# Kernel tuning notes

Measured on AMD Instinct MI355X. Metric: run time of the kernel, lower is better.

The kernel has to match this reference:

```python
import jax, jax.numpy as jnp
import numpy as np

QUANT_DEPTH = 4
EMBED_DIM = 256
N_EMBED = 8192
B, H, W = 8, 32, 32


def setup_inputs() -> dict:
    key = jax.random.key(0)
    k1, k2 = jax.random.split(key)
    x = jax.random.normal(k1, (B, H, W, EMBED_DIM), dtype=jnp.float32)
    codebooks = jax.random.normal(k2, (QUANT_DEPTH, N_EMBED, EMBED_DIM), dtype=jnp.float32)
    return {"x": x, "codebooks": codebooks}


def _nearest_code(flat, cb):
    # flat: [N, D], cb: [K, D] -> idx: [N]
    # ||v - c||^2 = ||v||^2 + ||c||^2 - 2 v.c  (addmm in torch source)
    d = (jnp.sum(flat * flat, axis=1, keepdims=True)
         + jnp.sum(cb * cb, axis=1)[None, :]
         - 2.0 * (flat @ cb.T))  # [N, K]
    return jnp.argmin(d, axis=1)


def reference(x, codebooks):
    Bx, h, w, D = x.shape
    # quantization path is entirely non-differentiable (torch: detach + no_grad)
    resid = jax.lax.stop_gradient(x)
    agg = jnp.zeros_like(resid)
    quant_list = []
    code_list = []
    for i in range(codebooks.shape[0]):
        cb = codebooks[i]                      # [K, D]
        idx = _nearest_code(resid.reshape(-1, D), cb)  # [N]
        quant = cb[idx].reshape(Bx, h, w, D)
        resid = resid - quant
        agg = agg + quant
        quant_list.append(agg)
        code_list.append(idx.reshape(Bx, h, w, 1))
    codes = jnp.concatenate(code_list, axis=-1)  # [B, h, w, depth]
    # commitment loss: mean over depths of mean((x - agg_i.detach())^2)
    commitment_loss = jnp.mean(
        jnp.stack([jnp.mean((x - jax.lax.stop_gradient(q)) ** 2) for q in quant_list]))
    # straight-through estimator
    quants_trunc = x + jax.lax.stop_gradient(quant_list[-1] - x)
    return quants_trunc, commitment_loss, codes
```

## Files before the change

### kernel.cpp

```cpp
#include <hip/hip_runtime.h>

#define DIM   256
#define NVEC  8192
#define NCODE 8192
#define DEPTH 4

#define KBLK  16
#define KC    (NCODE / KBLK)
#define FCAP  8192
#define FKS   32
#define FV    8
#define KAPPA 0.025f

typedef short  b8 __attribute__((ext_vector_type(8)));
typedef short  b4 __attribute__((ext_vector_type(4)));
typedef float  f4 __attribute__((ext_vector_type(4)));

static __device__ __forceinline__ unsigned short f2bf(float f) {
  unsigned u = __float_as_uint(f);
  return (unsigned short)((u + 0x7FFFu + ((u >> 16) & 1u)) >> 16);
}

static __device__ __forceinline__ void gll16(const void* g, void* l) {
  __builtin_amdgcn_global_load_lds(
      (const __attribute__((address_space(1))) void*)g,
      (__attribute__((address_space(3))) void*)l, 16, 0, 0);
}

__global__ __launch_bounds__(256) void prep_norms(const float* __restrict__ cb_all,
                                                  float* __restrict__ cc,
                                                  float* __restrict__ cchat) {
  int row  = blockIdx.x * 4 + (threadIdx.x >> 6);
  int lane = threadIdx.x & 63;
  float4 v = *(const float4*)&cb_all[(size_t)row * DIM + lane * 4];
  float st = 0.f, sh = 0.f;
  float vv[4] = {v.x, v.y, v.z, v.w};
  #pragma unroll
  for (int j = 0; j < 4; ++j) {
    float hf = __uint_as_float(((unsigned)f2bf(vv[j])) << 16);
    st += vv[j] * vv[j];
    sh += hf * hf;
  }
  #pragma unroll
  for (int off = 32; off > 0; off >>= 1) {
    st += __shfl_down(st, off, 64);
    sh += __shfl_down(sh, off, 64);
  }
  if (lane == 0) { cc[row] = st; cchat[row] = sh; }
}

__global__ __launch_bounds__(256) void prep_depth(const float* __restrict__ cbd,
                                                  unsigned short* __restrict__ cbh,
                                                  float* __restrict__ cbT) {
  __shared__ float ts[64][68];
  const int kb = blockIdx.x >> 2, db = blockIdx.x & 3;
  const int k0 = kb * 64, d0 = db * 64;
  const int t  = threadIdx.x;
  const int r  = t >> 2;
  const int c4 = (t & 3) * 16;

  const float* src = cbd + (size_t)(k0 + r) * DIM + d0 + c4;
  float4 q[4];
  #pragma unroll
  for (int i = 0; i < 4; ++i) q[i] = *(const float4*)(src + i * 4);

  b8 h0, h1;
  #pragma unroll
  for (int j = 0; j < 4; ++j) { h0[j] = (short)f2bf(q[0][j]); h0[4 + j] = (short)f2bf(q[1][j]); }
  #pragma unroll
  for (int j = 0; j < 4; ++j) { h1[j] = (short)f2bf(q[2][j]); h1[4 + j] = (short)f2bf(q[3][j]); }
  *(b8*)&cbh[(size_t)(k0 + r) * DIM + d0 + c4]     = h0;
  *(b8*)&cbh[(size_t)(k0 + r) * DIM + d0 + c4 + 8] = h1;

  #pragma unroll
  for (int i = 0; i < 4; ++i)
    #pragma unroll
    for (int j = 0; j < 4; ++j)
      ts[c4 + i * 4 + j][r] = q[i][j];
  __syncthreads();

  const int dd = t >> 2, kk4 = (t & 3) * 16;
  float* dst = cbT + (size_t)(d0 + dd) * NCODE + k0 + kk4;
  #pragma unroll
  for (int q4 = 0; q4 < 4; ++q4)
    *(float4*)(dst + q4 * 4) = *(const float4*)&ts[dd][kk4 + q4 * 4];
}

__global__ __launch_bounds__(256) void init_kernel(const float* __restrict__ x,
                                                   float* __restrict__ resid,
                                                   unsigned short* __restrict__ rb,
                                                   float* __restrict__ rsum0) {
  int n    = blockIdx.x * 4 + (threadIdx.x >> 6);
  int lane = threadIdx.x & 63;
  float4 v = *(const float4*)&x[(size_t)n * DIM + lane * 4];
  *(float4*)&resid[(size_t)n * DIM + lane * 4] = v;
  b4 hv; hv[0] = (short)f2bf(v.x); hv[1] = (short)f2bf(v.y);
  hv[2] = (short)f2bf(v.z); hv[3] = (short)f2bf(v.w);
  *(b4*)&rb[(size_t)n * DIM + lane * 4] = hv;
  float s = v.x * v.x + v.y * v.y + v.z * v.z + v.w * v.w;
  #pragma unroll
  for (int off = 32; off > 0; off >>= 1) s += __shfl_down(s, off, 64);
  if (lane == 0) rsum0[n] = s;
}

__global__ __launch_bounds__(512, 4) void coarse_kernel(
    const unsigned short* __restrict__ rb,
    const unsigned short* __restrict__ cbh,
    const float* __restrict__ cchat,
    float* __restrict__ pv1, int* __restrict__ pi1, float* __restrict__ pv2,
    int* __restrict__ fcount) {
  __shared__ __align__(16) char lds[65536];

  const int tid  = threadIdx.x;
  const int w    = tid >> 6;
  const int l    = tid & 63;
  const int mw   = w >> 1, kw = w & 1;
  const int mblk = blockIdx.x / KBLK;
  const int kblk = blockIdx.x % KBLK;
  const int m0   = mblk * 128;
  const int K0   = kblk * KC;

  if (blockIdx.x == 0 && tid == 0) *fcount = 0;

  int aoff[2], boff[2], ldst[2];
  #pragma unroll
  for (int it = 0; it < 2; ++it) {
    int o = it * 512 + tid;
    int row = o >> 3, ssl = (o & 7) ^ (row & 7);
    aoff[it] = (m0 + row) * 512 + ssl * 16;
    boff[it] = (K0 + row) * 512 + ssl * 16;
    ldst[it] = o * 16;
  }
  int offA[2][2], offB[4][2];
  #pragma unroll
  for (int mf = 0; mf < 2; ++mf) {
    int row = mw * 32 + mf * 16 + (l & 15);
    int base = row * 128 + (((l >> 4) ^ (row & 7)) * 16);
    offA[mf][0] = base; offA[mf][1] = base ^ 64;
  }
  #pragma unroll
  for (int nf = 0; nf < 4; ++nf) {
    int row = kw * 64 + nf * 16 + (l & 15);
    int base = row * 128 + (((l >> 4) ^ (row & 7)) * 16);
    offB[nf][0] = base; offB[nf][1] = base ^ 64;
  }

  const int kgb = K0 + kw * 64 + (l & 15);

  float tv1[8], tv2[8];
  int   ti1[8];
  #pragma unroll
  for (int s = 0; s < 8; ++s) { tv1[s] = 3.4e38f; tv2[s] = 3.4e38f; ti1[s] = 0; }

  f4 acc[2][4];

  #pragma unroll
  for (int it = 0; it < 2; ++it) {
    gll16((const char*)rb  + aoff[it], lds + ldst[it]);
    gll16((const char*)cbh + boff[it], lds + 16384 + ldst[it]);
  }
  __syncthreads();

  #pragma unroll 2
  for (int p = 0; p < 16; ++p) {
    const int buf = p & 1;
    const int kt  = p >> 2, dt = p & 3;
    if (p < 15) {
      const int np = p + 1;
      const int nb = np & 1, nkt = np >> 2, ndt = np & 3;
      #pragma unroll
      for (int it = 0; it < 2; ++it) {
        gll16((const char*)rb  + aoff[it] + ndt * 128,
              lds + nb * 32768 + ldst[it]);
        gll16((const char*)cbh + boff[it] + nkt * 65536 + ndt * 128,
              lds + nb * 32768 + 16384 + ldst[it]);
      }
    }
    if (dt == 0) {
      #pragma unroll
      for (int i = 0; i < 2; ++i)
        #pragma unroll
        for (int j = 0; j < 4; ++j)
          acc[i][j] = (f4){0.f, 0.f, 0.f, 0.f};
    }
    #pragma unroll
    for (int kk = 0; kk < 2; ++kk) {
      b8 af[2], bb[4];
      #pragma unroll
      for (int mf = 0; mf < 2; ++mf)
        af[mf] = *(const b8*)(lds + buf * 32768 + offA[mf][kk]);
      #pragma unroll
      for (int nf = 0; nf < 4; ++nf)
        bb[nf] = *(const b8*)(lds + buf * 32768 + 16384 + offB[nf][kk]);
      #pragma unroll
      for (int mf = 0; mf < 2; ++mf)
        #pragma unroll
        for (int nf = 0; nf < 4; ++nf)
          acc[mf][nf] = __builtin_amdgcn_mfma_f32_16x16x32_bf16(
              af[mf], bb[nf], acc[mf][nf], 0, 0, 0);
    }
    if (dt == 3) {
      float cn[4]; int kg[4];
      #pragma unroll
      for (int nf = 0; nf < 4; ++nf) {
        kg[nf] = kgb + kt * 128 + nf * 16;
        cn[nf] = cchat[kg[nf]];
      }
      #pragma unroll
      for (int mf = 0; mf < 2; ++mf)
        #pragma unroll
        for (int r = 0; r < 4; ++r) {
          const int s0 = mf * 4 + r;
          #pragma unroll
          for (int nf = 0; nf < 4; ++nf) {
            float s = fmaf(-2.f, acc[mf][nf][r], cn[nf]);
            bool  c = s < tv1[s0];
            float m2 = fminf(tv2[s0], s);
            tv2[s0] = c ? tv1[s0] : m2;
            ti1[s0] = c ? kg[nf] : ti1[s0];
            tv1[s0] = c ? s : tv1[s0];
          }
        }
    }
    __syncthreads();
  }

  float* Mv1 = (float*)lds;
  int*   Mi1 = (int*)(lds + 1024);
  float* Mv2 = (float*)(lds + 2048);

  #pragma unroll
  for (int s0 = 0; s0 < 8; ++s0) {
    float v1 = tv1[s0], v2 = tv2[s0];
    int   i1 = ti1[s0];
    #pragma unroll
    for (int m = 1; m < 16; m <<= 1) {
      float qv1 = __shfl_xor(v1, m);
      int   qi1 = __shfl_xor(i1, m);
      float qv2 = __shfl_xor(v2, m);
      bool  qw  = (qv1 < v1) || (qv1 == v1 && qi1 < i1);
      float lose = qw ? v1 : qv1;
      float wv2  = qw ? qv2 : v2;
      v2 = fminf(wv2, lose);
      if (qw) { v1 = qv1; i1 = qi1; }
    }
    if ((l & 15) == 0) {
      int mf = s0 >> 2, r = s0 & 3;
      int rowL = mw * 32 + mf * 16 + (l >> 4) * 4 + r;
      Mv1[rowL * 2 + kw] = v1; Mi1[rowL * 2 + kw] = i1; Mv2[rowL * 2 + kw] = v2;
    }
  }
  __syncthreads();
  if (tid < 128) {
    float a1 = Mv1[tid * 2],     a2 = Mv2[tid * 2];     int a1i = Mi1[tid * 2];
    float b1 = Mv1[tid * 2 + 1], b2 = Mv2[tid * 2 + 1]; int b1i = Mi1[tid * 2 + 1];
    bool  bw = (b1 < a1) || (b1 == a1 && b1i < a1i);
    float v1 = bw ? b1 : a1; int i1 = bw ? b1i : a1i;
    float v2 = fminf(bw ? b2 : a2, bw ? a1 : b1);
    int n = m0 + tid;
    pv1[kblk * NVEC + n] = v1;
    pi1[kblk * NVEC + n] = i1;
    pv2[kblk * NVEC + n] = v2;
  }
}

__global__ __launch_bounds__(256) void merge_kernel(
    const float* __restrict__ pv1, const int* __restrict__ pi1,
    const float* __restrict__ pv2, const float* __restrict__ vnorm,
    int* __restrict__ idx, int* __restrict__ flist, int* __restrict__ fslot,
    int* __restrict__ fcount) {
  int n = blockIdx.x * 256 + threadIdx.x;
  float v1 = 3.4e38f, v2 = 3.4e38f; int i1 = 0;
  #pragma unroll
  for (int kb = 0; kb < KBLK; ++kb) {
    float b1 = pv1[kb * NVEC + n]; int b1i = pi1[kb * NVEC + n];
    float b2 = pv2[kb * NVEC + n];
    bool  bw = (b1 < v1) || (b1 == v1 && b1i < i1);
    float lose = bw ? v1 : b1;
    float wv2  = bw ? b2 : v2;
    v2 = fminf(wv2, lose);
    if (bw) { v1 = b1; i1 = b1i; }
  }
  idx[n] = i1;
  float thr = KAPPA * sqrtf(fmaxf(v1 + vnorm[n], 0.f)) + 1e-5f;
  int slot = -1;
  if (v2 - v1 < thr) {
    slot = atomicAdd(fcount, 1);
    flist[slot] = n;
  }
  fslot[n] = slot;
}

__global__ __launch_bounds__(256, 4) void fb_scan_t(
    const float* __restrict__ cbT, const float* __restrict__ cc,
    const float* __restrict__ resid, const int* __restrict__ flist,
    const int* __restrict__ fcount,
    float* __restrict__ fpv, int* __restrict__ fpi) {
  __shared__ float vsT[DIM][FV + 4];
  __shared__ float mv[FV][4];
  __shared__ int   mi[FV][4];
  const int cnt = min(*fcount, FCAP);
  const int ks = blockIdx.x & (FKS - 1);
  const int t = threadIdx.x;
  const int w = t >> 6, l = t & 63;
  const int k = ks * 256 + t;
  const float cn = cc[k];

  for (int chunk = blockIdx.x >> 5; chunk * FV < cnt; chunk += 256) {
    __syncthreads();
    #pragma unroll
    for (int v = 0; v < FV; ++v) {
      int s = chunk * FV + v;
      int n = flist[s < cnt ? s : chunk * FV];
      vsT[t][v] = resid[(size_t)n * DIM + t];
    }
    __syncthreads();

    float dot[FV];
    #pragma unroll
    for (int v = 0; v < FV; ++v) dot[v] = 0.f;

    #pragma unroll 8
    for (int d = 0; d < DIM; ++d) {
      float cv = cbT[(size_t)d * NCODE + k];
      f4 a0 = *(const f4*)&vsT[d][0];
      f4 a1 = *(const f4*)&vsT[d][4];
      dot[0] = fmaf(cv, a0[0], dot[0]);
      dot[1] = fmaf(cv, a0[1], dot[1]);
      dot[2] = fmaf(cv, a0[2], dot[2]);
      dot[3] = fmaf(cv, a0[3], dot[3]);
      dot[4] = fmaf(cv, a1[0], dot[4]);
      dot[5] = fmaf(cv, a1[1], dot[5]);
      dot[6] = fmaf(cv, a1[2], dot[6]);
      dot[7] = fmaf(cv, a1[3], dot[7]);
    }

    #pragma unroll
    for (int v = 0; v < FV; ++v) {
      float bv = fmaf(-2.f, dot[v], cn);
      int   bi = k;
      #pragma unroll
      for (int m = 1; m < 64; m <<= 1) {
        float qv = __shfl_xor(bv, m);
        int   qi = __shfl_xor(bi, m);
        if (qv < bv || (qv == bv && qi < bi)) { bv = qv; bi = qi; }
      }
      if (l == 0) { mv[v][w] = bv; mi[v][w] = bi; }
    }
    __syncthreads();
    if (t < FV) {
      float bv = mv[t][0]; int bi = mi[t][0];
      #pragma unroll
      for (int ww = 1; ww < 4; ++ww) {
        float qv = mv[t][ww]; int qi = mi[t][ww];
        if (qv < bv || (qv == bv && qi < bi)) { bv = qv; bi = qi; }
      }
      if (chunk * FV + t < cnt) {
        fpv[(size_t)(chunk * FV + t) * FKS + ks] = bv;
        fpi[(size_t)(chunk * FV + t) * FKS + ks] = bi;
      }
    }
  }
}

__global__ __launch_bounds__(256) void update_kernel(
    const float* __restrict__ cb, const int* __restrict__ idx,
    const int* __restrict__ fslot,
    const float* __restrict__ fpv, const int* __restrict__ fpi,
    float* __restrict__ resid, unsigned short* __restrict__ rb,
    float* __restrict__ rsum_out, float* __restrict__ codes_out, int depth) {
  int n    = blockIdx.x * 4 + (threadIdx.x >> 6);
  int lane = threadIdx.x & 63;
  int s    = fslot[n];
  int bi;
  if (s >= 0) {
    float v = 3.4e38f; int ii = 0x7fffffff;
    if (lane < FKS) { v = fpv[(size_t)s * FKS + lane]; ii = fpi[(size_t)s * FKS + lane]; }
    #pragma unroll
    for (int m = 1; m < FKS; m <<= 1) {
      float qv = __shfl_xor(v, m);
      int   qi = __shfl_xor(ii, m);
      if (qv < v || (qv == v && qi < ii)) { v = qv; ii = qi; }
    }
    bi = __shfl(ii, 0, 64);
  } else {
    bi = idx[n];
  }
  float4 q = *(const float4*)&cb[(size_t)bi * DIM + lane * 4];
  float4 r = *(float4*)&resid[(size_t)n * DIM + lane * 4];
  r.x -= q.x; r.y -= q.y; r.z -= q.z; r.w -= q.w;
  *(float4*)&resid[(size_t)n * DIM + lane * 4] = r;
  b4 hv; hv[0] = (short)f2bf(r.x); hv[1] = (short)f2bf(r.y);
  hv[2] = (short)f2bf(r.z); hv[3] = (short)f2bf(r.w);
  *(b4*)&rb[(size_t)n * DIM + lane * 4] = hv;
  float s2 = r.x * r.x + r.y * r.y + r.z * r.z + r.w * r.w;
  #pragma unroll
  for (int off = 32; off > 0; off >>= 1) s2 += __shfl_down(s2, off, 64);
  if (lane == 0) {
    rsum_out[n] = s2;
    codes_out[n * DEPTH + depth] = (float)bi;
  }
}

__global__ __launch_bounds__(256) void finalize(const float* __restrict__ x,
                                                float* __restrict__ out,
                                                const float* __restrict__ rsumL) {
  int i = blockIdx.x * blockDim.x + threadIdx.x;
  float4 r  = *(float4*)&out[(size_t)i * 4];
  float4 xv = *(const float4*)&x[(size_t)i * 4];
  float4 o;
  o.x = xv.x - r.x; o.y = xv.y - r.y; o.z = xv.z - r.z; o.w = xv.w - r.w;
  *(float4*)&out[(size_t)i * 4] = o;

  if (blockIdx.x == 0) {
    __shared__ float sm[256];
    float s = 0.f;
    for (int j = threadIdx.x; j < DEPTH * NVEC; j += 256) s += rsumL[j];
    sm[threadIdx.x] = s;
    __syncthreads();
    for (int off = 128; off > 0; off >>= 1) {
      if (threadIdx.x < off) sm[threadIdx.x] += sm[threadIdx.x + off];
      __syncthreads();
    }
    if (threadIdx.x == 0)
      out[NVEC * DIM] = sm[0] / (float)DEPTH / (float)(NVEC * DIM);
  }
}

extern "C" void kernel_launch(void* const* d_in, const int* in_sizes, int n_in,
                              void* d_out, int out_size, void* d_ws, size_t ws_size,
                              hipStream_t stream) {
  const float* x  = (const float*)d_in[0];
  const float* cb = (const float*)d_in[1];
  float* out = (float*)d_out;
  char*  wsb = (char*)d_ws;

  unsigned short* cbh = (unsigned short*)(wsb);
  unsigned short* rb  = (unsigned short*)(wsb + 4194304);
  float* cbT   = (float*)(wsb + 8388608);
  float* cc    = (float*)(wsb + 16777216);
  float* cchat = (float*)(wsb + 16908288);
  float* pv1   = (float*)(wsb + 17039360);
  int*   pi1   = (int*)  (wsb + 17563648);
  float* pv2   = (float*)(wsb + 18087936);
  float* rsum  = (float*)(wsb + 18612224);
  int*   idx   = (int*)  (wsb + 18776064);
  int*   flist = (int*)  (wsb + 18808832);
  int*   fslot = (int*)  (wsb + 18841600);
  int*   fcount= (int*)  (wsb + 18874368);
  float* fpv   = (float*)(wsb + 18878464);
  int*   fpi   = (int*)  (wsb + 19927040);

  float* resid     = out;
  float* codes_out = out + NVEC * DIM + 1;

  prep_norms<<<(DEPTH * NCODE) / 4, 256, 0, stream>>>(cb, cc, cchat);
  init_kernel<<<NVEC / 4, 256, 0, stream>>>(x, resid, rb, rsum);

  for (int d = 0; d < DEPTH; ++d) {
    const size_t cbo = (size_t)d * NCODE * DIM;
    prep_depth<<<512, 256, 0, stream>>>(cb + cbo, cbh, cbT);
    coarse_kernel<<<(NVEC / 128) * KBLK, 512, 0, stream>>>(
        rb, cbh, cchat + d * NCODE, pv1, pi1, pv2, fcount);
    merge_kernel<<<NVEC / 256, 256, 0, stream>>>(
        pv1, pi1, pv2, rsum + d * NVEC, idx, flist, fslot, fcount);
    fb_scan_t<<<256 * FKS, 256, 0, stream>>>(
        cbT, cc + d * NCODE, resid, flist, fcount, fpv, fpi);
    update_kernel<<<NVEC / 4, 256, 0, stream>>>(
        cb + cbo, idx, fslot, fpv, fpi, resid, rb,
        rsum + (d + 1) * NVEC, codes_out, d);
  }
  finalize<<<(NVEC * DIM / 4) / 256, 256, 0, stream>>>(x, out, rsum + NVEC);
}
```

Measured before the change: 528.2 us.

## Keep residual A fragments in registers and halve code-block split count

```diff
diff --git a/kernel.cpp b/kernel.cpp
--- a/kernel.cpp
+++ b/kernel.cpp
@@ -5,8 +5,9 @@
 #define NCODE 8192
 #define DEPTH 4
 
-#define KBLK  16
+#define KBLK  8
 #define KC    (NCODE / KBLK)
+#define KT    (KC / 128)
 #define FCAP  8192
 #define FKS   32
 #define FV    8
@@ -153,6 +154,7 @@
   for (int s = 0; s < 8; ++s) { tv1[s] = 3.4e38f; tv2[s] = 3.4e38f; ti1[s] = 0; }
 
   f4 acc[2][4];
+  b8 ar[4][2][2];
 
   #pragma unroll
   for (int it = 0; it < 2; ++it) {
@@ -161,68 +163,80 @@
   }
   __syncthreads();
 
-  #pragma unroll 2
-  for (int p = 0; p < 16; ++p) {
-    const int buf = p & 1;
-    const int kt  = p >> 2, dt = p & 3;
-    if (p < 15) {
-      const int np = p + 1;
-      const int nb = np & 1, nkt = np >> 2, ndt = np & 3;
+  for (int kt = 0; kt < KT; ++kt) {
+    #pragma unroll
+    for (int dt = 0; dt < 4; ++dt) {
+      const int buf = dt & 1;
+      if (!(kt == KT - 1 && dt == 3)) {
+        const int ndt = (dt + 1) & 3;
+        const int nb  = ndt & 1;
+        const int nktoff = (dt == 3) ? (kt + 1) * 65536 : kt * 65536;
+        if (kt == 0 && dt < 3) {
+          #pragma unroll
+          for (int it = 0; it < 2; ++it)
+            gll16((const char*)rb + aoff[it] + ndt * 128,
+                  lds + nb * 32768 + ldst[it]);
+        }
+        #pragma unroll
+        for (int it = 0; it < 2; ++it)
+          gll16((const char*)cbh + boff[it] + nktoff + ndt * 128,
+                lds + nb * 32768 + 16384 + ldst[it]);
+      }
+      if (dt == 0) {
+        #pragma unroll
+        for (int i = 0; i < 2; ++i)
+          #pragma unroll
+          for (int j = 0; j < 4; ++j)
+            acc[i][j] = (f4){0.f, 0.f, 0.f, 0.f};
+      }
       #pragma unroll
-      for (int it = 0; it < 2; ++it) {
-        gll16((const char*)rb  + aoff[it] + ndt * 128,
-              lds + nb * 32768 + ldst[it]);
-        gll16((const char*)cbh + boff[it] + nkt * 65536 + ndt * 128,
-              lds + nb * 32768 + 16384 + ldst[it]);
-      }
-    }
-    if (dt == 0) {
-      #pragma unroll
-      for (int i = 0; i < 2; ++i)
-        #pragma unroll
-        for (int j = 0; j < 4; ++j)
-          acc[i][j] = (f4){0.f, 0.f, 0.f, 0.f};
-    }
-    #pragma unroll
-    for (int kk = 0; kk < 2; ++kk) {
-      b8 af[2], bb[4];
-      #pragma unroll
-      for (int mf = 0; mf < 2; ++mf)
-        af[mf] = *(const b8*)(lds + buf * 32768 + offA[mf][kk]);
-      #pragma unroll
-      for (int nf = 0; nf < 4; ++nf)
-        bb[nf] = *(const b8*)(lds + buf * 32768 + 16384 + offB[nf][kk]);
-      #pragma unroll
-      for (int mf = 0; mf < 2; ++mf)
+      for (int kk = 0; kk < 2; ++kk) {
+        b8 af[2], bb[4];
+        if (kt == 0) {
+          #pragma unroll
+          for (int mf = 0; mf < 2; ++mf) {
+            af[mf] = *(const b8*)(lds + buf * 32768 + offA[mf][kk]);
+            ar[dt][kk][mf] = af[mf];
+          }
+        } else {
+          #pragma unroll
+          for (int mf = 0; mf < 2; ++mf) af[mf] = ar[dt][kk][mf];
+        }
         #pragma unroll
         for (int nf = 0; nf < 4; ++nf)
-          acc[mf][nf] = __builtin_amdgcn_mfma_f32_16x16x32_bf16(
-              af[mf], bb[nf], acc[mf][nf], 0, 0, 0);
-    }
-    if (dt == 3) {
-      float cn[4]; int kg[4];
-      #pragma unroll
-      for (int nf = 0; nf < 4; ++nf) {
-        kg[nf] = kgb + kt * 128 + nf * 16;
-        cn[nf] = cchat[kg[nf]];
-      }
-      #pragma unroll
-      for (int mf = 0; mf < 2; ++mf)
-        #pragma unroll
-        for (int r = 0; r < 4; ++r) {
-          const int s0 = mf * 4 + r;
-          #pragma unroll
-          for (int nf = 0; nf < 4; ++nf) {
-            float s = fmaf(-2.f, acc[mf][nf][r], cn[nf]);
-            bool  c = s < tv1[s0];
-            float m2 = fminf(tv2[s0], s);
-            tv2[s0] = c ? tv1[s0] : m2;
-            ti1[s0] = c ? kg[nf] : ti1[s0];
-            tv1[s0] = c ? s : tv1[s0];
+          bb[nf] = *(const b8*)(lds + buf * 32768 + 16384 + offB[nf][kk]);
+        #pragma unroll
+        for (int mf = 0; mf < 2; ++mf)
+          #pragma unroll
+          for (int nf = 0; nf < 4; ++nf)
+            acc[mf][nf] = __builtin_amdgcn_mfma_f32_16x16x32_bf16(
+                af[mf], bb[nf], acc[mf][nf], 0, 0, 0);
+      }
+      if (dt == 3) {
+        float cn[4]; int kg[4];
+        #pragma unroll
+        for (int nf = 0; nf < 4; ++nf) {
+          kg[nf] = kgb + kt * 128 + nf * 16;
+          cn[nf] = cchat[kg[nf]];
+        }
+        #pragma unroll
+        for (int mf = 0; mf < 2; ++mf)
+          #pragma unroll
+          for (int r = 0; r < 4; ++r) {
+            const int s0 = mf * 4 + r;
+            #pragma unroll
+            for (int nf = 0; nf < 4; ++nf) {
+              float s = fmaf(-2.f, acc[mf][nf][r], cn[nf]);
+              bool  c = s < tv1[s0];
+              float m2 = fminf(tv2[s0], s);
+              tv2[s0] = c ? tv1[s0] : m2;
+              ti1[s0] = c ? kg[nf] : ti1[s0];
+              tv1[s0] = c ? s : tv1[s0];
+            }
           }
-        }
-    }
-    __syncthreads();
+      }
+      __syncthreads();
+    }
   }
 
   float* Mv1 = (float*)lds;
```

Result: slower. 619.9 us (+17.4%).
